# Kernel tuning notes

Measured on AMD Instinct MI355X. Metric: run time of the kernel, lower is better.

Reference implementation:

```python
import jax, jax.numpy as jnp
import numpy as np

B, S, D = 2, 4096, 256
H, KD = 8, 256  # keras MHA built with key_dim=d_model -> per-head dim = 256
DFF = 1024
EPS = 1e-3  # keras LayerNormalization default epsilon
NEG = 1e9


def setup_inputs() -> dict:
    key = jax.random.key(0)
    ks = jax.random.split(key, 16)
    sd = 0.02
    return {
        "x": jax.random.normal(ks[0], (B, S, D), jnp.float32),
        "w_2": 128,
        "Wq": jax.random.normal(ks[1], (D, H, KD), jnp.float32) * sd,
        "bq": jnp.zeros((H, KD), jnp.float32),
        "Wk": jax.random.normal(ks[2], (D, H, KD), jnp.float32) * sd,
        "bk": jnp.zeros((H, KD), jnp.float32),
        "Wv": jax.random.normal(ks[3], (D, H, KD), jnp.float32) * sd,
        "bv": jnp.zeros((H, KD), jnp.float32),
        "Wo": jax.random.normal(ks[4], (H, KD, D), jnp.float32) * sd,
        "bo": jnp.zeros((D,), jnp.float32),
        "W1": jax.random.normal(ks[5], (D, DFF), jnp.float32) * sd,
        "b1": jnp.zeros((DFF,), jnp.float32),
        "W2": jax.random.normal(ks[6], (DFF, D), jnp.float32) * sd,
        "b2": jnp.zeros((D,), jnp.float32),
        "g1": jnp.ones((D,), jnp.float32),
        "be1": jnp.zeros((D,), jnp.float32),
        "g2": jnp.ones((D,), jnp.float32),
        "be2": jnp.zeros((D,), jnp.float32),
    }


def layer_norm(x, g, b):
    mu = jnp.mean(x, axis=-1, keepdims=True)
    var = jnp.mean(jnp.square(x - mu), axis=-1, keepdims=True)
    return (x - mu) * jax.lax.rsqrt(var + EPS) * g + b


def reference(x, w_2, Wq, bq, Wk, bk, Wv, bv, Wo, bo, W1, b1, W2, b2, g1, be1, g2, be2):
    # --- sliding-window self attention (dense scores + mask, as in source) ---
    q = jnp.einsum('bsd,dhk->bshk', x, Wq) + bq
    k = jnp.einsum('bsd,dhk->bshk', x, Wk) + bk
    v = jnp.einsum('bsd,dhk->bshk', x, Wv) + bv
    scores = jnp.einsum('bqhd,bkhd->bhqk', q, k) / jnp.sqrt(jnp.asarray(KD, x.dtype))
    idx = jnp.arange(S)
    mask = (jnp.abs(idx[:, None] - idx[None, :]) <= w_2)  # [S, S]
    scores = scores + (1.0 - mask.astype(x.dtype)) * (-NEG)
    attn = jax.nn.softmax(scores, axis=-1)
    ctx = jnp.einsum('bhqk,bkhd->bqhd', attn, v)
    attn_out = jnp.einsum('bqhd,hdo->bqo', ctx, Wo) + bo
    x = layer_norm(x + attn_out, g1, be1)
    # --- feed-forward ---
    h = jax.nn.relu(jnp.einsum('bsd,df->bsf', x, W1) + b1)
    ffn = jnp.einsum('bsf,fd->bsd', h, W2) + b2
    x = layer_norm(x + ffn, g2, be2)
    return x
```

## Files before the change

### kernel.cpp

```cpp
#include <hip/hip_runtime.h>
#include <hip/hip_bf16.h>

#define Bn 2
#define Sn 4096
#define Dn 256
#define Hn 8
#define KDn 256
#define DFFn 1024
#define Mn (Bn*Sn)
#define NQKVn (Hn*KDn)

typedef __attribute__((ext_vector_type(4))) float f32x4;
typedef __attribute__((ext_vector_type(8))) short bf16x8;
typedef __attribute__((ext_vector_type(4))) short short4v;

__device__ __forceinline__ short f2bf(float f) {
  unsigned u = __builtin_bit_cast(unsigned, f);
  unsigned r = u + 0x7fffu + ((u >> 16) & 1u);
  return (short)(r >> 16);
}

#define GLL16(gsrc, ldst) \
  __builtin_amdgcn_global_load_lds((const __attribute__((address_space(1))) void*)(gsrc), \
                                   (__attribute__((address_space(3))) void*)(ldst), 16, 0, 0)

__global__ __launch_bounds__(256)
void cvt_x(const float* __restrict__ x, short* __restrict__ xb, int n) {
  int i = (blockIdx.x * 256 + threadIdx.x) * 4;
  if (i < n) {
    float4 v = *(const float4*)(x + i);
    short4v o = { f2bf(v.x), f2bf(v.y), f2bf(v.z), f2bf(v.w) };
    *(short4v*)(xb + i) = o;
  }
}

__global__ __launch_bounds__(256)
void concat_bias(const float* __restrict__ bq, const float* __restrict__ bk,
                 const float* __restrict__ bv, float* __restrict__ o) {
  int i = blockIdx.x * 256 + threadIdx.x;
  o[i] = (i < 2048) ? bq[i] : (i < 4096 ? bk[i - 2048] : bv[i - 4096]);
}

__global__ __launch_bounds__(256)
void cvt_weights(const float* __restrict__ Wq, const float* __restrict__ Wk,
                 const float* __restrict__ Wv, const float* __restrict__ Wo,
                 const float* __restrict__ W1, const float* __restrict__ W2,
                 short* __restrict__ WqT, short* __restrict__ WkT,
                 short* __restrict__ WvT, short* __restrict__ WoT,
                 short* __restrict__ W1T, short* __restrict__ W2T) {
  int t = blockIdx.x;
  const float* W; short* WT; int K, N;
  if      (t < 512)  { W = Wq; WT = WqT; K = 256;  N = 2048; }
  else if (t < 1024) { t -= 512;  W = Wk; WT = WkT; K = 256;  N = 2048; }
  else if (t < 1536) { t -= 1024; W = Wv; WT = WvT; K = 256;  N = 2048; }
  else if (t < 2048) { t -= 1536; W = Wo; WT = WoT; K = 2048; N = 256;  }
  else if (t < 2304) { t -= 2048; W = W1; WT = W1T; K = 256;  N = 1024; }
  else               { t -= 2304; W = W2; WT = W2T; K = 1024; N = 256;  }
  const int ktiles = K >> 5;
  const int k0 = (t % ktiles) * 32, n0 = (t / ktiles) * 32;
  __shared__ short tt[32][33];
  const int tx = threadIdx.x & 31, ty = threadIdx.x >> 5;
#pragma unroll
  for (int i = 0; i < 32; i += 8)
    tt[ty + i][tx] = f2bf(W[(size_t)(k0 + ty + i) * N + n0 + tx]);
  __syncthreads();
#pragma unroll
  for (int i = 0; i < 32; i += 8)
    WT[(size_t)(n0 + ty + i) * K + k0 + tx] = tt[tx][ty + i];
}

__global__ __launch_bounds__(256, 2)
void gemm_qkv(const short* __restrict__ A, const short* __restrict__ BT,
              const float* __restrict__ bias, short* __restrict__ Qo,
              short* __restrict__ Ko, short* __restrict__ Vto) {
  __shared__ __align__(16) short smem[16640];
  short* As = smem;
  short* Bs = smem + 4096;
  const int tid = threadIdx.x;
  const int lane = tid & 63;
  const int wave = tid >> 6;
  const int tn = blockIdx.x;
  const int tm = blockIdx.y;
  const int wr = (wave >> 1) * 64;
  const int wc = (wave & 1) * 64;
  const int lrow = lane & 15;
  const int lk = (lane >> 4) * 8;
  const int K = 256;

  f32x4 acc[4][4];
#pragma unroll
  for (int i = 0; i < 4; ++i)
#pragma unroll
    for (int j = 0; j < 4; ++j) acc[i][j] = (f32x4){0.f, 0.f, 0.f, 0.f};

  const int row_s = tid >> 2;
  const int col_s = (tid & 3) * 8;
  const short* aS = A + (size_t)(tm * 128 + row_s) * K + col_s;
  const short* bS = BT + (size_t)(tn * 128 + row_s) * K + col_s;
  short* AsB = As + wave * 512;
  short* BsB = Bs + wave * 512;

  for (int kt = 0; kt < 8; ++kt) {
    GLL16(aS, AsB);
    GLL16(aS + (size_t)64 * K, AsB + 2048);
    GLL16(bS, BsB);
    GLL16(bS + (size_t)64 * K, BsB + 2048);
    aS += 32; bS += 32;
    __syncthreads();
    bf16x8 af[4], bfr[4];
#pragma unroll
    for (int i = 0; i < 4; ++i) {
      af[i]  = *(const bf16x8*)(As + (wr + i * 16 + lrow) * 32 + lk);
      bfr[i] = *(const bf16x8*)(Bs + (wc + i * 16 + lrow) * 32 + lk);
    }
#pragma unroll
    for (int i = 0; i < 4; ++i)
#pragma unroll
      for (int j = 0; j < 4; ++j)
        acc[i][j] = __builtin_amdgcn_mfma_f32_16x16x32_bf16(af[i], bfr[j], acc[i][j], 0, 0, 0);
    __syncthreads();
  }

  const int rbase = (lane >> 4) * 4;
  if (tn < 32) {
    short* C = (tn < 16) ? Qo : Ko;
    const float sc = (tn < 16) ? 1.f : 0.0625f;
    const int cb = (tn & 15) * 128;
#pragma unroll
    for (int j = 0; j < 4; ++j) {
      const int cj = wc + j * 16 + lrow;
      const float bv = bias[tn * 128 + cj];
      const int cl = cb + cj;
#pragma unroll
      for (int i = 0; i < 4; ++i) {
        const int row0 = tm * 128 + wr + i * 16 + rbase;
        f32x4 a = acc[i][j];
#pragma unroll
        for (int r = 0; r < 4; ++r)
          C[(size_t)(row0 + r) * NQKVn + cl] = f2bf((a[r] + bv) * sc);
      }
    }
  } else {
    __syncthreads();
    short* Ct = smem;
#pragma unroll
    for (int j = 0; j < 4; ++j) {
      const int colL = wc + j * 16 + lrow;
      const float bv = bias[tn * 128 + colL];
#pragma unroll
      for (int i = 0; i < 4; ++i) {
        const int rowL0 = wr + i * 16 + rbase;
        f32x4 a = acc[i][j];
        short4v o = { f2bf(a[0] + bv), f2bf(a[1] + bv), f2bf(a[2] + bv), f2bf(a[3] + bv) };
        *(short4v*)(&Ct[colL * 130 + rowL0]) = o;
      }
    }
    __syncthreads();
    const int kd_l = tid >> 1;
    const int so = (tid & 1) * 64;
    const int cl = (tn - 32) * 128 + kd_l;
    const int hh = cl >> 8;
    const int kd = cl & 255;
    const int row0 = tm * 128;
    const int bb = row0 >> 12;
    const int s0 = (row0 & (Sn - 1)) + so;
    short* dst = Vto + (size_t)((bb * Hn + hh) * KDn + kd) * Sn + s0;
#pragma unroll
    for (int u = 0; u < 64; u += 8)
      *(bf16x8*)(dst + u) = *(const bf16x8*)(&Ct[kd_l * 130 + so + u]);
  }
}

__global__ __launch_bounds__(256, 2)
void gemm_ffn1(const short* __restrict__ A, const short* __restrict__ BT,
               const float* __restrict__ bias, short* __restrict__ C,
               int N, int K) {
  __shared__ __align__(16) short As[128 * 32];
  __shared__ __align__(16) short Bs[128 * 32];
  const int tid = threadIdx.x;
  const int lane = tid & 63;
  const int wave = tid >> 6;
  const int tn = blockIdx.x;
  const int tm = blockIdx.y;
  const int wr = (wave >> 1) * 64;
  const int wc = (wave & 1) * 64;
  const int lrow = lane & 15;
  const int lk = (lane >> 4) * 8;

  f32x4 acc[4][4];
#pragma unroll
  for (int i = 0; i < 4; ++i)
#pragma unroll
    for (int j = 0; j < 4; ++j) acc[i][j] = (f32x4){0.f, 0.f, 0.f, 0.f};

  const int row_s = tid >> 2;
  const int col_s = (tid & 3) * 8;
  const short* aS = A + (size_t)(tm * 128 + row_s) * K + col_s;
  const short* bS = BT + (size_t)(tn * 128 + row_s) * K + col_s;
  short* AsB = As + wave * 512;
  short* BsB = Bs + wave * 512;

  const int nk = K >> 5;
  for (int kt = 0; kt < nk; ++kt) {
    GLL16(aS, AsB);
    GLL16(aS + (size_t)64 * K, AsB + 2048);
    GLL16(bS, BsB);
    GLL16(bS + (size_t)64 * K, BsB + 2048);
    aS += 32; bS += 32;
    __syncthreads();
    bf16x8 af[4], bfr[4];
#pragma unroll
    for (int i = 0; i < 4; ++i) {
      af[i]  = *(const bf16x8*)(As + (wr + i * 16 + lrow) * 32 + lk);
      bfr[i] = *(const bf16x8*)(Bs + (wc + i * 16 + lrow) * 32 + lk);
    }
#pragma unroll
    for (int i = 0; i < 4; ++i)
#pragma unroll
      for (int j = 0; j < 4; ++j)
        acc[i][j] = __builtin_amdgcn_mfma_f32_16x16x32_bf16(af[i], bfr[j], acc[i][j], 0, 0, 0);
    __syncthreads();
  }

  const int rbase = (lane >> 4) * 4;
#pragma unroll
  for (int j = 0; j < 4; ++j) {
    const int col = tn * 128 + wc + j * 16 + lrow;
    const float bv = bias[col];
#pragma unroll
    for (int i = 0; i < 4; ++i) {
      const int row0 = tm * 128 + wr + i * 16 + rbase;
      f32x4 a = acc[i][j];
#pragma unroll
      for (int r = 0; r < 4; ++r)
        C[(size_t)(row0 + r) * N + col] = f2bf(fmaxf(a[r] + bv, 0.f));
    }
  }
}

__global__ __launch_bounds__(256, 4)
void gemm_bt64(const short* __restrict__ A, const short* __restrict__ BT,
               const float* __restrict__ bias, float* __restrict__ C,
               int N, int K) {
  __shared__ __align__(16) short As[64 * 32];
  __shared__ __align__(16) short Bs[64 * 32];
  const int tid = threadIdx.x;
  const int lane = tid & 63;
  const int wave = tid >> 6;
  const int tn = blockIdx.x;
  const int tm = blockIdx.y;
  const int wr = (wave >> 1) * 32;
  const int wc = (wave & 1) * 32;
  const int lrow = lane & 15;
  const int lk = (lane >> 4) * 8;

  f32x4 acc[2][2];
#pragma unroll
  for (int i = 0; i < 2; ++i)
#pragma unroll
    for (int j = 0; j < 2; ++j) acc[i][j] = (f32x4){0.f, 0.f, 0.f, 0.f};

  const int row_s = tid >> 2;
  const int col_s = (tid & 3) * 8;
  const short* aS = A + (size_t)(tm * 64 + row_s) * K + col_s;
  const short* bS = BT + (size_t)(tn * 64 + row_s) * K + col_s;
  short* AsB = As + wave * 512;
  short* BsB = Bs + wave * 512;

  const int nk = K >> 5;
  for (int kt = 0; kt < nk; ++kt) {
    GLL16(aS, AsB);
    GLL16(bS, BsB);
    aS += 32; bS += 32;
    __syncthreads();
    bf16x8 af[2], bfr[2];
#pragma unroll
    for (int i = 0; i < 2; ++i) {
      af[i]  = *(const bf16x8*)(As + (wr + i * 16 + lrow) * 32 + lk);
      bfr[i] = *(const bf16x8*)(Bs + (wc + i * 16 + lrow) * 32 + lk);
    }
#pragma unroll
    for (int i = 0; i < 2; ++i)
#pragma unroll
      for (int j = 0; j < 2; ++j)
        acc[i][j] = __builtin_amdgcn_mfma_f32_16x16x32_bf16(af[i], bfr[j], acc[i][j], 0, 0, 0);
    __syncthreads();
  }

  const int rbase = (lane >> 4) * 4;
#pragma unroll
  for (int j = 0; j < 2; ++j) {
    const int col = tn * 64 + wc + j * 16 + lrow;
    const float bv = bias[col];
#pragma unroll
    for (int i = 0; i < 2; ++i) {
      const int row0 = tm * 64 + wr + i * 16 + rbase;
      f32x4 a = acc[i][j];
#pragma unroll
      for (int r = 0; r < 4; ++r) C[(size_t)(row0 + r) * N + col] = a[r] + bv;
    }
  }
}

__global__ __launch_bounds__(512, 1)
void attn_win(const short* __restrict__ q, const short* __restrict__ k,
              const short* __restrict__ vt, short* __restrict__ ctx,
              const int* __restrict__ w2p) {
  const int bid = blockIdx.x;
  const int swz = (bid & 7) * 32 + (bid >> 3);
  const int q0 = (swz & 15) * 256;
  const int h = (swz >> 4) & 7;
  const int b = swz >> 7;
  const int tid = threadIdx.x;
  const int lane = tid & 63;
  const int wave = tid >> 6;
  const int w2 = *w2p;
  const int qw = q0 + wave * 32;
  const int lrow = lane & 15;
  const int lk = (lane >> 4) * 8;
  const int lk2 = lk * 2;
  const int rbase = (lane >> 4) * 4;

  __shared__ __align__(16) short Ks[3][8192];
  __shared__ __align__(16) short Vs[3][8192];
  __shared__ __align__(16) short Ps[8][1024];
  short* P = Ps[wave];

  const short* qbase = q + (size_t)(b * Sn + qw) * NQKVn + h * KDn;
  bf16x8 qf[2][8];
#pragma unroll
  for (int mi = 0; mi < 2; ++mi)
#pragma unroll
    for (int ks = 0; ks < 8; ++ks)
      qf[mi][ks] = *(const bf16x8*)(qbase + (size_t)(mi * 16 + lrow) * NQKVn + ks * 32 + lk);

  f32x4 oacc[2][16];
#pragma unroll
  for (int mi = 0; mi < 2; ++mi)
#pragma unroll
    for (int nc = 0; nc < 16; ++nc) oacc[mi][nc] = (f32x4){0.f, 0.f, 0.f, 0.f};

  float lsum[2][4];
#pragma unroll
  for (int mi = 0; mi < 2; ++mi)
#pragma unroll
    for (int r = 0; r < 4; ++r) lsum[mi][r] = 0.f;

  const short* kbase = k + (size_t)(b * Sn) * NQKVn + h * KDn;
  const short* vtb = vt + (size_t)((b * Hn + h) * KDn) * Sn;

  int bstart = q0 - w2; if (bstart < 0) bstart = 0; bstart &= ~31;
  int bend = q0 + 256 + w2; if (bend > Sn) bend = Sn; bend = (bend + 31) & ~31;
  int wlo = qw - w2; if (wlo < 0) wlo = 0; wlo &= ~31;
  int whi = qw + 32 + w2; if (whi > Sn) whi = Sn;

  auto stage = [&](int c0, int bf) {
#pragma unroll
    for (int e = 0; e < 2; ++e) {
      const int o = e * 8192 + tid * 16;
      const int row = o >> 9;
      const int cc = (o & 511) ^ ((row & 7) << 4);
      GLL16(kbase + (size_t)(c0 + row) * NQKVn + (cc >> 1),
            (char*)Ks[bf] + e * 8192 + wave * 1024);
    }
#pragma unroll
    for (int e = 0; e < 2; ++e) {
      const int o = e * 8192 + tid * 16;
      const int row = o >> 6;
      const int cc = (o & 63) ^ ((row & 3) << 4);
      GLL16(vtb + (size_t)row * Sn + c0 + (cc >> 1),
            (char*)Vs[bf] + e * 8192 + wave * 1024);
    }
  };

  const int nch = (bend - bstart) >> 5;
  stage(bstart, 0);
  if (nch > 1) stage(bstart + 32, 1);

  int cur = 0;
  for (int i = 0; i < nch; ++i) {
    const int c0 = bstart + i * 32;
    if (i + 2 < nch) stage(c0 + 64, (cur + 2 >= 3) ? cur - 1 : cur + 2);
    if (i == 0) {
      asm volatile("s_waitcnt vmcnt(0)" ::: "memory");
    } else {
      const int ahead = ((i + 3 < nch) ? i + 3 : nch) - i - 1;
      if (ahead >= 2)      asm volatile("s_waitcnt vmcnt(8)" ::: "memory");
      else if (ahead == 1) asm volatile("s_waitcnt vmcnt(4)" ::: "memory");
      else                 asm volatile("s_waitcnt vmcnt(0)" ::: "memory");
    }
    __builtin_amdgcn_s_barrier();
    asm volatile("" ::: "memory");

    if (c0 >= wlo && c0 < whi) {
      const char* Kc = (const char*)Ks[cur];
      const int x0 = (lrow & 7) << 4;
      f32x4 sf[2][2];
      sf[0][0] = sf[0][1] = sf[1][0] = sf[1][1] = (f32x4){0.f, 0.f, 0.f, 0.f};
#pragma unroll
      for (int ks = 0; ks < 8; ++ks) {
        const int cb = (lk2 + ks * 64) ^ x0;
        bf16x8 kf0 = *(const bf16x8*)(Kc + lrow * 512 + cb);
        bf16x8 kf1 = *(const bf16x8*)(Kc + (16 + lrow) * 512 + cb);
        sf[0][0] = __builtin_amdgcn_mfma_f32_16x16x32_bf16(qf[0][ks], kf0, sf[0][0], 0, 0, 0);
        sf[0][1] = __builtin_amdgcn_mfma_f32_16x16x32_bf16(qf[0][ks], kf1, sf[0][1], 0, 0, 0);
        sf[1][0] = __builtin_amdgcn_mfma_f32_16x16x32_bf16(qf[1][ks], kf0, sf[1][0], 0, 0, 0);
        sf[1][1] = __builtin_amdgcn_mfma_f32_16x16x32_bf16(qf[1][ks], kf1, sf[1][1], 0, 0, 0);
      }
      const bool full = (c0 >= qw + 31 - w2) && (c0 + 31 <= qw + w2);
      if (full) {
#pragma unroll
        for (int mi = 0; mi < 2; ++mi)
#pragma unroll
          for (int ni = 0; ni < 2; ++ni)
#pragma unroll
            for (int r = 0; r < 4; ++r) {
              const float p = __expf(sf[mi][ni][r]);
              sf[mi][ni][r] = p;
              lsum[mi][r] += p;
            }
      } else {
#pragma unroll
        for (int mi = 0; mi < 2; ++mi)
#pragma unroll
          for (int ni = 0; ni < 2; ++ni) {
            const int kk = c0 + ni * 16 + lrow;
#pragma unroll
            for (int r = 0; r < 4; ++r) {
              const int dd = (qw + mi * 16 + rbase + r) - kk;
              const bool val = (dd <= w2) && (dd >= -w2);
              float p = __expf(sf[mi][ni][r]);
              p = val ? p : 0.f;
              sf[mi][ni][r] = p;
              lsum[mi][r] += p;
            }
          }
      }
#pragma unroll
      for (int mi = 0; mi < 2; ++mi)
#pragma unroll
        for (int ni = 0; ni < 2; ++ni)
#pragma unroll
          for (int r = 0; r < 4; ++r)
            P[(mi * 16 + rbase + r) * 32 + ni * 16 + lrow] = f2bf(sf[mi][ni][r]);

      bf16x8 pa0 = *(const bf16x8*)(P + lrow * 32 + lk);
      bf16x8 pa1 = *(const bf16x8*)(P + (16 + lrow) * 32 + lk);
      const char* Vc = (const char*)Vs[cur] + lrow * 64 + (lk2 ^ ((lrow & 3) << 4));
#pragma unroll
      for (int nc = 0; nc < 16; ++nc) {
        bf16x8 vf = *(const bf16x8*)(Vc + nc * 1024);
        oacc[0][nc] = __builtin_amdgcn_mfma_f32_16x16x32_bf16(pa0, vf, oacc[0][nc], 0, 0, 0);
        oacc[1][nc] = __builtin_amdgcn_mfma_f32_16x16x32_bf16(pa1, vf, oacc[1][nc], 0, 0, 0);
      }
    }
    cur = (cur == 2) ? 0 : cur + 1;
  }

#pragma unroll
  for (int mi = 0; mi < 2; ++mi)
#pragma unroll
    for (int r = 0; r < 4; ++r) {
      float s = lsum[mi][r];
#pragma unroll
      for (int d = 1; d < 16; d <<= 1) s += __shfl_xor(s, d);
      lsum[mi][r] = 1.f / s;
    }

  short* cbase = ctx + (size_t)(b * Sn + qw) * NQKVn + h * KDn;
#pragma unroll
  for (int mi = 0; mi < 2; ++mi)
#pragma unroll
    for (int nc = 0; nc < 16; ++nc)
#pragma unroll
      for (int r = 0; r < 4; ++r)
        cbase[(size_t)(mi * 16 + rbase + r) * NQKVn + nc * 16 + lrow] =
            f2bf(oacc[mi][nc][r] * lsum[mi][r]);
}

__global__ __launch_bounds__(256)
void ln_fused(const float* __restrict__ xin, const float* __restrict__ yin,
              const float* __restrict__ g, const float* __restrict__ bb,
              float* __restrict__ of32, short* __restrict__ obf) {
  const int row = blockIdx.x * 4 + (threadIdx.x >> 6);
  const int lane = threadIdx.x & 63;
  const size_t base = (size_t)row * Dn + lane * 4;
  float4 a = *(const float4*)(xin + base);
  float4 bv = *(const float4*)(yin + base);
  float4 v = { a.x + bv.x, a.y + bv.y, a.z + bv.z, a.w + bv.w };
  float sum = v.x + v.y + v.z + v.w;
  float ssq = v.x * v.x + v.y * v.y + v.z * v.z + v.w * v.w;
#pragma unroll
  for (int d = 1; d < 64; d <<= 1) { sum += __shfl_xor(sum, d); ssq += __shfl_xor(ssq, d); }
  const float mu = sum * (1.f / Dn);
  const float var = ssq * (1.f / Dn) - mu * mu;
  const float rs = rsqrtf(var + 1e-3f);
  float4 gg = *(const float4*)(g + lane * 4);
  float4 bbv = *(const float4*)(bb + lane * 4);
  float4 o = { (v.x - mu) * rs * gg.x + bbv.x, (v.y - mu) * rs * gg.y + bbv.y,
               (v.z - mu) * rs * gg.z + bbv.z, (v.w - mu) * rs * gg.w + bbv.w };
  if (of32) *(float4*)(of32 + base) = o;
  if (obf) {
    short4v ob = { f2bf(o.x), f2bf(o.y), f2bf(o.z), f2bf(o.w) };
    *(short4v*)(obf + base) = ob;
  }
}

extern "C" void kernel_launch(void* const* d_in, const int* in_sizes, int n_in,
                              void* d_out, int out_size, void* d_ws, size_t ws_size,
                              hipStream_t stream) {
  const float* x   = (const float*)d_in[0];
  const int*   w2p = (const int*)d_in[1];
  const float* Wq  = (const float*)d_in[2];
  const float* bq  = (const float*)d_in[3];
  const float* Wk  = (const float*)d_in[4];
  const float* bk  = (const float*)d_in[5];
  const float* Wv  = (const float*)d_in[6];
  const float* bv  = (const float*)d_in[7];
  const float* Wo  = (const float*)d_in[8];
  const float* bo  = (const float*)d_in[9];
  const float* W1  = (const float*)d_in[10];
  const float* b1  = (const float*)d_in[11];
  const float* W2  = (const float*)d_in[12];
  const float* b2  = (const float*)d_in[13];
  const float* g1  = (const float*)d_in[14];
  const float* be1 = (const float*)d_in[15];
  const float* g2  = (const float*)d_in[16];
  const float* be2 = (const float*)d_in[17];
  float* out = (float*)d_out;

  char* ws = (char*)d_ws;
  size_t off = 0;
  auto alloc = [&](size_t bytes) { void* p = ws + off; off += (bytes + 255) & ~(size_t)255; return p; };
  short* xb    = (short*)alloc((size_t)Mn * Dn * 2);
  short* WqkvT = (short*)alloc((size_t)3 * NQKVn * Dn * 2);
  float* bqkv  = (float*)alloc((size_t)3 * NQKVn * 4);
  short* WoT   = (short*)alloc((size_t)Dn * NQKVn * 2);
  short* W1T   = (short*)alloc((size_t)DFFn * Dn * 2);
  short* W2T   = (short*)alloc((size_t)Dn * DFFn * 2);
  short* qb    = (short*)alloc((size_t)Mn * NQKVn * 2);
  short* kb    = (short*)alloc((size_t)Mn * NQKVn * 2);
  short* vtb   = (short*)alloc((size_t)Mn * NQKVn * 2);
  float* attn_out = (float*)alloc((size_t)Mn * Dn * 4);
  float* x1    = (float*)alloc((size_t)Mn * Dn * 4);
  short* ctxb = qb;
  short* x1b  = xb;
  short* hb   = kb;
  float* ffn  = attn_out;

  cvt_x<<<dim3(Mn * Dn / 1024), dim3(256), 0, stream>>>(x, xb, Mn * Dn);
  cvt_weights<<<dim3(2560), dim3(256), 0, stream>>>(
      Wq, Wk, Wv, Wo, W1, W2,
      WqkvT, WqkvT + (size_t)NQKVn * Dn, WqkvT + (size_t)2 * NQKVn * Dn,
      WoT, W1T, W2T);
  concat_bias<<<dim3(24), dim3(256), 0, stream>>>(bq, bk, bv, bqkv);

  gemm_qkv<<<dim3(48, 64), dim3(256), 0, stream>>>(xb, WqkvT, bqkv, qb, kb, vtb);

  attn_win<<<dim3(256), dim3(512), 0, stream>>>(qb, kb, vtb, ctxb, w2p);

  gemm_bt64<<<dim3(Dn / 64, Mn / 64), dim3(256), 0, stream>>>(ctxb, WoT, bo, attn_out, Dn, NQKVn);
  ln_fused<<<dim3(Mn / 4), dim3(256), 0, stream>>>(x, attn_out, g1, be1, x1, x1b);
  gemm_ffn1<<<dim3(DFFn / 128, Mn / 128), dim3(256), 0, stream>>>(x1b, W1T, b1, hb, DFFn, Dn);
  gemm_bt64<<<dim3(Dn / 64, Mn / 64), dim3(256), 0, stream>>>(hb, W2T, b2, ffn, Dn, DFFn);
  ln_fused<<<dim3(Mn / 4), dim3(256), 0, stream>>>(x1, ffn, g2, be2, out, (short*)nullptr);
}
```

Measured before the change: 185.0 us.

## Triple-buffer GEMM K-loops with async LDS loads and single barrier

The QKV, FFN1 and bt64 GEMMs now stage global-to-LDS loads two k-tiles ahead into a three-slot ring. Each iteration uses one vmcnt wait plus one barrier instead of two __syncthreads, so load latency can overlap with MFMA work. The attention kernel's prefetch is moved after the barrier with a simpler vmcnt schedule. In exchange, LDS per block grows and occupancy hints rise to 3, and the hand-set vmcnt counts must match the number of loads issued per stage.

```diff
diff --git a/kernel.cpp b/kernel.cpp
--- a/kernel.cpp
+++ b/kernel.cpp
@@ -23,6 +23,11 @@
 #define GLL16(gsrc, ldst) \
   __builtin_amdgcn_global_load_lds((const __attribute__((address_space(1))) void*)(gsrc), \
                                    (__attribute__((address_space(3))) void*)(ldst), 16, 0, 0)
+
+#define WAITCNT4 asm volatile("s_waitcnt vmcnt(4)" ::: "memory")
+#define WAITCNT2 asm volatile("s_waitcnt vmcnt(2)" ::: "memory")
+#define WAITCNT0 asm volatile("s_waitcnt vmcnt(0)" ::: "memory")
+#define BARRIER  do { __builtin_amdgcn_s_barrier(); asm volatile("" ::: "memory"); } while (0)
 
 __global__ __launch_bounds__(256)
 void cvt_x(const float* __restrict__ x, short* __restrict__ xb, int n) {
@@ -69,13 +74,11 @@
     WT[(size_t)(n0 + ty + i) * K + k0 + tx] = tt[tx][ty + i];
 }
 
-__global__ __launch_bounds__(256, 2)
+__global__ __launch_bounds__(256, 3)
 void gemm_qkv(const short* __restrict__ A, const short* __restrict__ BT,
               const float* __restrict__ bias, short* __restrict__ Qo,
               short* __restrict__ Ko, short* __restrict__ Vto) {
-  __shared__ __align__(16) short smem[16640];
-  short* As = smem;
-  short* Bs = smem + 4096;
+  __shared__ __align__(16) short smem[3 * 8192];
   const int tid = threadIdx.x;
   const int lane = tid & 63;
   const int wave = tid >> 6;
@@ -85,7 +88,6 @@
   const int wc = (wave & 1) * 64;
   const int lrow = lane & 15;
   const int lk = (lane >> 4) * 8;
-  const int K = 256;
 
   f32x4 acc[4][4];
 #pragma unroll
@@ -95,18 +97,29 @@
 
   const int row_s = tid >> 2;
   const int col_s = (tid & 3) * 8;
-  const short* aS = A + (size_t)(tm * 128 + row_s) * K + col_s;
-  const short* bS = BT + (size_t)(tn * 128 + row_s) * K + col_s;
-  short* AsB = As + wave * 512;
-  short* BsB = Bs + wave * 512;
-
+  const short* aB = A + (size_t)(tm * 128 + row_s) * 256 + col_s;
+  const short* bB = BT + (size_t)(tn * 128 + row_s) * 256 + col_s;
+
+  auto stage = [&](int kt, int bf) {
+    const short* aP = aB + kt * 32;
+    const short* bP = bB + kt * 32;
+    short* AsB = smem + bf * 8192 + wave * 512;
+    short* BsB = smem + bf * 8192 + 4096 + wave * 512;
+    GLL16(aP, AsB);
+    GLL16(aP + 64 * 256, AsB + 2048);
+    GLL16(bP, BsB);
+    GLL16(bP + 64 * 256, BsB + 2048);
+  };
+
+  stage(0, 0);
+  stage(1, 1);
+  int cur = 0;
   for (int kt = 0; kt < 8; ++kt) {
-    GLL16(aS, AsB);
-    GLL16(aS + (size_t)64 * K, AsB + 2048);
-    GLL16(bS, BsB);
-    GLL16(bS + (size_t)64 * K, BsB + 2048);
-    aS += 32; bS += 32;
-    __syncthreads();
+    if (kt == 7) WAITCNT0; else WAITCNT4;
+    BARRIER;
+    if (kt + 2 < 8) { int nb = cur + 2; if (nb >= 3) nb -= 3; stage(kt + 2, nb); }
+    const short* As = smem + cur * 8192;
+    const short* Bs = As + 4096;
     bf16x8 af[4], bfr[4];
 #pragma unroll
     for (int i = 0; i < 4; ++i) {
@@ -118,7 +131,7 @@
 #pragma unroll
       for (int j = 0; j < 4; ++j)
         acc[i][j] = __builtin_amdgcn_mfma_f32_16x16x32_bf16(af[i], bfr[j], acc[i][j], 0, 0, 0);
-    __syncthreads();
+    ++cur; if (cur == 3) cur = 0;
   }
 
   const int rbase = (lane >> 4) * 4;
@@ -171,12 +184,11 @@
   }
 }
 
-__global__ __launch_bounds__(256, 2)
+__global__ __launch_bounds__(256, 3)
 void gemm_ffn1(const short* __restrict__ A, const short* __restrict__ BT,
                const float* __restrict__ bias, short* __restrict__ C,
                int N, int K) {
-  __shared__ __align__(16) short As[128 * 32];
-  __shared__ __align__(16) short Bs[128 * 32];
+  __shared__ __align__(16) short smem[3 * 8192];
   const int tid = threadIdx.x;
   const int lane = tid & 63;
   const int wave = tid >> 6;
@@ -195,19 +207,30 @@
 
   const int row_s = tid >> 2;
   const int col_s = (tid & 3) * 8;
-  const short* aS = A + (size_t)(tm * 128 + row_s) * K + col_s;
-  const short* bS = BT + (size_t)(tn * 128 + row_s) * K + col_s;
-  short* AsB = As + wave * 512;
-  short* BsB = Bs + wave * 512;
+  const short* aB = A + (size_t)(tm * 128 + row_s) * K + col_s;
+  const short* bB = BT + (size_t)(tn * 128 + row_s) * K + col_s;
+
+  auto stage = [&](int kt, int bf) {
+    const short* aP = aB + kt * 32;
+    const short* bP = bB + kt * 32;
+    short* AsB = smem + bf * 8192 + wave * 512;
+    short* BsB = smem + bf * 8192 + 4096 + wave * 512;
+    GLL16(aP, AsB);
+    GLL16(aP + (size_t)64 * K, AsB + 2048);
+    GLL16(bP, BsB);
+    GLL16(bP + (size_t)64 * K, BsB + 2048);
+  };
 
   const int nk = K >> 5;
+  stage(0, 0);
+  if (nk > 1) stage(1, 1);
+  int cur = 0;
   for (int kt = 0; kt < nk; ++kt) {
-    GLL16(aS, AsB);
-    GLL16(aS + (size_t)64 * K, AsB + 2048);
-    GLL16(bS, BsB);
-    GLL16(bS + (size_t)64 * K, BsB + 2048);
-    aS += 32; bS += 32;
-    __syncthreads();
+    if (kt == nk - 1) WAITCNT0; else WAITCNT4;
+    BARRIER;
+    if (kt + 2 < nk) { int nb = cur + 2; if (nb >= 3) nb -= 3; stage(kt + 2, nb); }
+    const short* As = smem + cur * 8192;
+    const short* Bs = As + 4096;
     bf16x8 af[4], bfr[4];
 #pragma unroll
     for (int i = 0; i < 4; ++i) {
@@ -219,7 +242,7 @@
 #pragma unroll
       for (int j = 0; j < 4; ++j)
         acc[i][j] = __builtin_amdgcn_mfma_f32_16x16x32_bf16(af[i], bfr[j], acc[i][j], 0, 0, 0);
-    __syncthreads();
+    ++cur; if (cur == 3) cur = 0;
   }
 
   const int rbase = (lane >> 4) * 4;
@@ -242,8 +265,7 @@
 void gemm_bt64(const short* __restrict__ A, const short* __restrict__ BT,
                const float* __restrict__ bias, float* __restrict__ C,
                int N, int K) {
-  __shared__ __align__(16) short As[64 * 32];
-  __shared__ __align__(16) short Bs[64 * 32];
+  __shared__ __align__(16) short smem[3 * 4096];
   const int tid = threadIdx.x;
   const int lane = tid & 63;
   const int wave = tid >> 6;
@@ -262,17 +284,24 @@
 
   const int row_s = tid >> 2;
   const int col_s = (tid & 3) * 8;
-  const short* aS = A + (size_t)(tm * 64 + row_s) * K + col_s;
-  const short* bS = BT + (size_t)(tn * 64 + row_s) * K + col_s;
-  short* AsB = As + wave * 512;
-  short* BsB = Bs + wave * 512;
+  const short* aB = A + (size_t)(tm * 64 + row_s) * K + col_s;
+  const short* bB = BT + (size_t)(tn * 64 + row_s) * K + col_s;
+
+  auto stage = [&](int kt, int bf) {
+    GLL16(aB + kt * 32, smem + bf * 4096 + wave * 512);
+    GLL16(bB + kt * 32, smem + bf * 4096 + 2048 + wave * 512);
+  };
 
   const int nk = K >> 5;
+  stage(0, 0);
+  if (nk > 1) stage(1, 1);
+  int cur = 0;
   for (int kt = 0; kt < nk; ++kt) {
-    GLL16(aS, AsB);
-    GLL16(bS, BsB);
-    aS += 32; bS += 32;
-    __syncthreads();
+    if (kt == nk - 1) WAITCNT0; else WAITCNT2;
+    BARRIER;
+    if (kt + 2 < nk) { int nb = cur + 2; if (nb >= 3) nb -= 3; stage(kt + 2, nb); }
+    const short* As = smem + cur * 4096;
+    const short* Bs = As + 2048;
     bf16x8 af[2], bfr[2];
 #pragma unroll
     for (int i = 0; i < 2; ++i) {
@@ -284,7 +313,7 @@
 #pragma unroll
       for (int j = 0; j < 2; ++j)
         acc[i][j] = __builtin_amdgcn_mfma_f32_16x16x32_bf16(af[i], bfr[j], acc[i][j], 0, 0, 0);
-    __syncthreads();
+    ++cur; if (cur == 3) cur = 0;
   }
 
   const int rbase = (lane >> 4) * 4;
@@ -380,17 +409,9 @@
   int cur = 0;
   for (int i = 0; i < nch; ++i) {
     const int c0 = bstart + i * 32;
-    if (i + 2 < nch) stage(c0 + 64, (cur + 2 >= 3) ? cur - 1 : cur + 2);
-    if (i == 0) {
-      asm volatile("s_waitcnt vmcnt(0)" ::: "memory");
-    } else {
-      const int ahead = ((i + 3 < nch) ? i + 3 : nch) - i - 1;
-      if (ahead >= 2)      asm volatile("s_waitcnt vmcnt(8)" ::: "memory");
-      else if (ahead == 1) asm volatile("s_waitcnt vmcnt(4)" ::: "memory");
-      else                 asm volatile("s_waitcnt vmcnt(0)" ::: "memory");
-    }
-    __builtin_amdgcn_s_barrier();
-    asm volatile("" ::: "memory");
+    if (i == nch - 1) WAITCNT0; else WAITCNT4;
+    BARRIER;
+    if (i + 2 < nch) { int nb = cur + 2; if (nb >= 3) nb -= 3; stage(c0 + 64, nb); }
 
     if (c0 >= wlo && c0 < whi) {
       const char* Kc = (const char*)Ks[cur];
@@ -454,7 +475,7 @@
         oacc[1][nc] = __builtin_amdgcn_mfma_f32_16x16x32_bf16(pa1, vf, oacc[1][nc], 0, 0, 0);
       }
     }
-    cur = (cur == 2) ? 0 : cur + 1;
+    ++cur; if (cur == 3) cur = 0;
   }
 
 #pragma unroll
```

Measured after the change: 187.5 us. Within noise of the previous version (+1.3%).
